# Performance work log

Hardware: AMD Instinct MI355X
Metric: run time of the kernel (lower is better)

## Reference

```python
import jax, jax.numpy as jnp
import numpy as np

WS = 7          # window size
NH = 12         # num heads
DIM = 384
HD = DIM // NH  # head dim = 32
EPS = 1e-5


def _ln(x, g, b):
    m = x.mean(-1, keepdims=True)
    v = ((x - m) ** 2).mean(-1, keepdims=True)
    return (x - m) / jnp.sqrt(v + EPS) * g + b


def _rel_index():
    # exact replica of WindowAttention.__init__ relative_position_index
    coords = np.stack(np.meshgrid(np.arange(WS), np.arange(WS), indexing='ij'))  # (2,ws,ws)
    flat = coords.reshape(2, -1)                                                 # (2,49)
    rel = flat[:, :, None] - flat[:, None, :]                                    # (2,49,49)
    rel = rel.transpose(1, 2, 0).astype(np.int32)
    rel[:, :, 0] += WS - 1
    rel[:, :, 1] += WS - 1
    rel[:, :, 0] *= 2 * WS - 1
    return jnp.asarray(rel.sum(-1))  # (49,49), values in [0, 169)


def setup_inputs() -> dict:
    key = jax.random.key(0)
    ks = jax.random.split(key, 16)
    B, H, W = 16, 56, 56
    L = H * W
    hidden = int(DIM * 4.0)
    p = lambda k, shp: (jax.random.normal(k, shp, jnp.float32) * 0.02)
    return {
        'x': jax.random.normal(ks[0], (B, L, DIM), jnp.float32),
        'kv': jax.random.normal(ks[1], (2, B, NH, WS * WS, HD), jnp.float32),
        'rel_index': _rel_index(),
        'H': H, 'W': W,
        'g1': jnp.ones((DIM,), jnp.float32), 'b1': jnp.zeros((DIM,), jnp.float32),
        'Wqkv': p(ks[2], (DIM, 3 * DIM)), 'bqkv': jnp.zeros((3 * DIM,), jnp.float32),
        'bias_table': p(ks[3], ((2 * WS - 1) ** 2, NH)),
        'Wproj': p(ks[4], (DIM, DIM)), 'bproj': jnp.zeros((DIM,), jnp.float32),
        'g2': jnp.ones((DIM,), jnp.float32), 'b2': jnp.zeros((DIM,), jnp.float32),
        'Wfc1': p(ks[5], (DIM, hidden)), 'bfc1': jnp.zeros((hidden,), jnp.float32),
        'Wfc2': p(ks[6], (hidden, DIM)), 'bfc2': jnp.zeros((DIM,), jnp.float32),
    }


def reference(x, kv, rel_index, H, W, g1, b1, Wqkv, bqkv, bias_table, Wproj, bproj,
              g2, b2, Wfc1, bfc1, Wfc2, bfc2):
    B, L, C = x.shape
    scale = HD ** -0.5
    nWh, nWw = H // WS, W // WS  # H,W divisible by WS -> pad is a no-op; shift_size=0 -> no roll/mask

    h = _ln(x, g1, b1).reshape(B, H, W, C)
    # window_partition -> (B*nW, N, C), N = WS*WS
    hw = h.reshape(B, nWh, WS, nWw, WS, C).transpose(0, 1, 3, 2, 4, 5).reshape(-1, WS * WS, C)
    B_, N, _ = hw.shape

    qkv = (hw @ Wqkv + bqkv).reshape(B_, N, 3, NH, HD).transpose(2, 0, 3, 1, 4)  # (3,B_,nh,N,hd)
    q = qkv[0] * scale
    k, v = kv[0], kv[1]                     # (B, nh, num_kv, hd)
    reps = B_ // k.shape[0]
    k = jnp.repeat(k, reps, axis=0)         # repeat_interleave: each image's windows share its kv
    v = jnp.repeat(v, reps, axis=0)

    attn = jnp.einsum('bhqd,bhkd->bhqk', q, k)                      # (B_,nh,N,N)
    bias = bias_table[rel_index.reshape(-1)].reshape(N, N, NH).transpose(2, 0, 1)
    attn = jax.nn.softmax(attn + bias[None], axis=-1)
    o = jnp.einsum('bhqk,bhkd->bhqd', attn, v)                      # (B_,nh,N,hd)
    o = o.transpose(0, 2, 1, 3).reshape(B_, N, C) @ Wproj + bproj

    # window_reverse -> (B, L, C)
    o = o.reshape(B, nWh, nWw, WS, WS, C).transpose(0, 1, 3, 2, 4, 5).reshape(B, L, C)
    x = x + o
    x = x + (jax.nn.gelu(_ln(x, g2, b2) @ Wfc1 + bfc1, approximate=False) @ Wfc2 + bfc2)
    return x
```

## Files before the change

kernel.cpp:

```cpp
#include <hip/hip_runtime.h>

typedef __attribute__((ext_vector_type(8))) short short8;
typedef __attribute__((ext_vector_type(4))) float floatx4;
typedef unsigned int u32;

#define DIM 384
#define NHEAD 12
#define HDIM 32

__device__ __forceinline__ float bf2f(unsigned int u) {
    union { unsigned int i; float f; } x; x.i = (u & 0xffffu) << 16; return x.f;
}
__device__ __forceinline__ unsigned short f2bf(float f) {
    union { float f; unsigned int i; } x; x.f = f;
    return (unsigned short)((x.i + 0x7fffu + ((x.i >> 16) & 1u)) >> 16);
}

__device__ __forceinline__ int nat2win(int r) {
    int b = r / 3136; int l = r - b * 3136;
    int hh = l / 56, wc = l - hh * 56;
    int wh = hh / 7, nr = hh - wh * 7;
    int ww = wc / 7, nc = wc - ww * 7;
    return ((b << 6) + wh * 8 + ww) * 49 + nr * 7 + nc;
}
__device__ __forceinline__ int win2nat(int r) {
    int w = r / 49; int n = r - w * 49;
    int b = w >> 6; int wi = w & 63;
    int wh = wi >> 3, ww = wi & 7;
    int hh = wh * 7 + n / 7, wc = ww * 7 + n % 7;
    return b * 3136 + hh * 56 + wc;
}

#define GLOAD_LDS16(g, l) \
    __builtin_amdgcn_global_load_lds((const __attribute__((address_space(1))) u32*)(g), \
                                     (__attribute__((address_space(3))) u32*)(l), 16, 0, 0)

#define LDS_U32(p) ((u32)(uintptr_t)(__attribute__((address_space(3))) unsigned short*)(p))

template <int OFF>
__device__ __forceinline__ short8 ds_read128(u32 addr) {
    short8 r;
    asm volatile("ds_read_b128 %0, %1 offset:%2" : "=v"(r) : "v"(addr), "i"(OFF));
    return r;
}

__global__ void transpose_kernel(const float* __restrict__ src,
                                 unsigned short* __restrict__ dst,
                                 int K, int N, int ld) {
    int i = blockIdx.x * blockDim.x + threadIdx.x;
    if (i >= K * N) return;
    int n = i / K, k = i - n * K;
    dst[i] = f2bf(src[(size_t)k * ld + n]);
}

__global__ void bias_expand_kernel(const int* __restrict__ rel_index,
                                   const float* __restrict__ bias_table,
                                   float* __restrict__ biasx) {
    int i = blockIdx.x * blockDim.x + threadIdx.x;
    if (i >= NHEAD * 49 * 49) return;
    int h = i / 2401, r = i - h * 2401;
    biasx[i] = bias_table[rel_index[r] * NHEAD + h];
}

__global__ __launch_bounds__(64) void ln_kernel(const float* __restrict__ x,
                                                const float* __restrict__ g,
                                                const float* __restrict__ b,
                                                unsigned short* __restrict__ out,
                                                int windowed) {
    int r = blockIdx.x;
    int lane = threadIdx.x;
    const float* row = x + (size_t)r * DIM;
    float v[6];
    float s = 0.f, ss = 0.f;
#pragma unroll
    for (int j = 0; j < 3; j++) {
        int c = lane + j * 64;
        float2 f = *(const float2*)(row + 2 * c);
        v[2 * j] = f.x; v[2 * j + 1] = f.y;
        s += f.x + f.y; ss += f.x * f.x + f.y * f.y;
    }
#pragma unroll
    for (int m = 1; m < 64; m <<= 1) {
        s += __shfl_xor(s, m);
        ss += __shfl_xor(ss, m);
    }
    float mean = s * (1.f / DIM);
    float var = ss * (1.f / DIM) - mean * mean;
    float rstd = rsqrtf(var + 1e-5f);
    int orow = windowed ? nat2win(r) : r;
    unsigned short* op = out + (size_t)orow * DIM;
#pragma unroll
    for (int j = 0; j < 3; j++) {
        int c = lane + j * 64;
        float2 gg = *(const float2*)(g + 2 * c);
        float2 bb = *(const float2*)(b + 2 * c);
        float o0 = (v[2 * j] - mean) * rstd * gg.x + bb.x;
        float o1 = (v[2 * j + 1] - mean) * rstd * gg.y + bb.y;
        unsigned int w = ((unsigned int)f2bf(o1) << 16) | f2bf(o0);
        *(unsigned int*)(op + 2 * c) = w;
    }
}

__global__ __launch_bounds__(256) void attn_kernel(const unsigned short* __restrict__ q,
                                                   const float* __restrict__ kv,
                                                   const float* __restrict__ biasx,
                                                   unsigned short* __restrict__ o) {
    __shared__ alignas(16) unsigned short Ks[64 * 40];
    __shared__ alignas(16) unsigned short Vt[32 * 72];
    __shared__ float Bi[49 * 52];
    __shared__ alignas(16) unsigned short Ps[4][16 * 72];

    int blk = blockIdx.x;
    int b = blk / 48; int rem = blk - b * 48;
    int h = rem >> 2; int g = rem & 3;
    size_t row_base = (size_t)(b * 64 + g * 16) * 49;

    int t = threadIdx.x;
    int lane = t & 63;
    int wv = t >> 6;
    int lr = lane & 15;
    int lg = lane >> 4;

    const float* kptr = kv + (size_t)(b * NHEAD + h) * 1568;
    for (int idx = t; idx < 392; idx += 256) {
        int row = idx >> 3, seg = idx & 7;
        float4 f = *(const float4*)(kptr + row * 32 + seg * 4);
        ushort4 h4; h4.x = f2bf(f.x); h4.y = f2bf(f.y); h4.z = f2bf(f.z); h4.w = f2bf(f.w);
        *(ushort4*)&Ks[row * 40 + seg * 4] = h4;
    }
    const float* vptr = kv + (size_t)(192 + b * NHEAD + h) * 1568;
    for (int idx = t; idx < 784; idx += 256) {
        int m = idx >> 4, dp = idx & 15;
        float2 f = *(const float2*)(vptr + m * 32 + dp * 2);
        Vt[(2 * dp) * 72 + m]     = f2bf(f.x);
        Vt[(2 * dp + 1) * 72 + m] = f2bf(f.y);
    }
    for (int idx = t; idx < 32 * 23; idx += 256) {
        int d = idx / 23, m = 49 + idx - d * 23;
        Vt[d * 72 + m] = 0;
    }
    const float* bh = biasx + h * 2401;
    for (int idx = t; idx < 2401; idx += 256) {
        int qr = idx / 49, k = idx - qr * 49;
        Bi[qr * 52 + k] = bh[idx];
    }
    __syncthreads();

    short8 bfr[4], vbf[2][2];
#pragma unroll
    for (int ni = 0; ni < 4; ni++)
        bfr[ni] = *(const short8*)&Ks[(ni * 16 + lr) * 40 + lg * 8];
#pragma unroll
    for (int ni = 0; ni < 2; ni++)
#pragma unroll
        for (int ks = 0; ks < 2; ks++)
            vbf[ni][ks] = *(const short8*)&Vt[(ni * 16 + lr) * 72 + ks * 32 + lg * 8];

    const unsigned short* qb = q + row_base * DIM + h * 32 + lg * 8;
    unsigned short* ob = o + row_base * DIM + h * 32;

    short8 af = *(const short8*)(qb + (size_t)(wv * 16 + lr) * DIM);
    for (int tm = wv; tm < 49; tm += 4) {
        short8 af_next;
        if (tm + 4 < 49) af_next = *(const short8*)(qb + (size_t)((tm + 4) * 16 + lr) * DIM);

        floatx4 sfrag[4];
#pragma unroll
        for (int ni = 0; ni < 4; ni++)
            sfrag[ni] = __builtin_amdgcn_mfma_f32_16x16x32_bf16(af, bfr[ni], (floatx4)0.f, 0, 0, 0);

#pragma unroll
        for (int reg = 0; reg < 4; reg++) {
            int r_loc = tm * 16 + lg * 4 + reg;
            int qr = r_loc % 49;
            float mx = -1e30f;
#pragma unroll
            for (int ni = 0; ni < 4; ni++) {
                int k = ni * 16 + lr;
                float s = sfrag[ni][reg];
                if (k < 49) s += Bi[qr * 52 + k];
                else s = -1e30f;
                sfrag[ni][reg] = s;
                mx = fmaxf(mx, s);
            }
#pragma unroll
            for (int j = 1; j < 16; j <<= 1) mx = fmaxf(mx, __shfl_xor(mx, j));
            float sum = 0.f;
#pragma unroll
            for (int ni = 0; ni < 4; ni++) {
                float e = __expf(sfrag[ni][reg] - mx);
                sfrag[ni][reg] = e;
                sum += e;
            }
#pragma unroll
            for (int j = 1; j < 16; j <<= 1) sum += __shfl_xor(sum, j);
            float inv = 1.f / sum;
#pragma unroll
            for (int ni = 0; ni < 4; ni++)
                Ps[wv][(lg * 4 + reg) * 72 + ni * 16 + lr] = f2bf(sfrag[ni][reg] * inv);
        }
        floatx4 ofrag[2] = {(floatx4)0.f, (floatx4)0.f};
#pragma unroll
        for (int ks = 0; ks < 2; ks++) {
            short8 paf = *(const short8*)&Ps[wv][lr * 72 + ks * 32 + lg * 8];
#pragma unroll
            for (int ni = 0; ni < 2; ni++)
                ofrag[ni] = __builtin_amdgcn_mfma_f32_16x16x32_bf16(paf, vbf[ni][ks], ofrag[ni], 0, 0, 0);
        }
#pragma unroll
        for (int reg = 0; reg < 4; reg++) {
            size_t rg = (size_t)(tm * 16 + lg * 4 + reg) * DIM;
#pragma unroll
            for (int ni = 0; ni < 2; ni++)
                ob[rg + ni * 16 + lr] = f2bf(ofrag[ni][reg]);
        }
        af = af_next;
    }
}

template <int DO_GELU, int DO_REMAP, int OUT_BF16>
__global__ __launch_bounds__(256) void gemm_kernel(const unsigned short* __restrict__ A,
                                                   const unsigned short* __restrict__ Bt,
                                                   const float* __restrict__ bias,
                                                   const float* __restrict__ res,
                                                   void* __restrict__ outv,
                                                   int M, int N, int K, float scale) {
    __shared__ alignas(16) unsigned short As[3][128 * 32];
    __shared__ alignas(16) unsigned short Bs[2][128 * 32];

    int nwg = gridDim.x * gridDim.y;
    int lid = blockIdx.y * gridDim.x + blockIdx.x;
    int q8 = nwg >> 3, r8 = nwg & 7;
    int xcd = lid & 7, pos = lid >> 3;
    int nlid = (xcd < r8 ? xcd * (q8 + 1) : r8 * (q8 + 1) + (xcd - r8) * q8) + pos;
    int m0 = (nlid / gridDim.x) * 128;
    int n0 = (nlid % gridDim.x) * 128;

    int t = threadIdx.x;
    int lane = t & 63;
    int wv = t >> 6;
    int wm = (wv >> 1) * 64, wn = (wv & 1) * 64;
    int lr = lane & 15;
    int lq = lane >> 4;

    int rowS = t >> 2;
    int pcS = t & 3;
    int xrS = (rowS & 3) ^ ((rowS >> 2) & 3);
    int gcS = ((pcS ^ xrS) << 3);

    int xrR = (lr & 3) ^ ((lr >> 2) & 3);
    int swB = ((lq ^ xrR) << 4);

    floatx4 acc[4][4];
#pragma unroll
    for (int i = 0; i < 4; i++)
#pragma unroll
        for (int j = 0; j < 4; j++) acc[i][j] = (floatx4)0.f;

    const unsigned short* Abase = A + (size_t)(m0 + rowS) * K + gcS;
    const unsigned short* Bbase = Bt + (size_t)(n0 + rowS) * K + gcS;
    size_t rstep = (size_t)64 * K;

    auto stageA = [&](int buf, int kk) {
        GLOAD_LDS16(Abase + kk, &As[buf][t * 8]);
        GLOAD_LDS16(Abase + rstep + kk, &As[buf][(256 + t) * 8]);
    };
    auto stageB = [&](int buf, int kk) {
        GLOAD_LDS16(Bbase + kk, &Bs[buf][t * 8]);
        GLOAD_LDS16(Bbase + rstep + kk, &Bs[buf][(256 + t) * 8]);
    };

    u32 asBase = LDS_U32(&As[0][0]);
    u32 bsBase = LDS_U32(&Bs[0][0]);
    u32 aRow = (u32)(((wm + lr) * 64)) + (u32)swB;
    u32 bRow = (u32)(((wn + lr) * 64)) + (u32)swB;

    const int nk = K >> 5;

    stageB(0, 0);
    stageA(0, 0);
    stageA(1, 32);

    for (int kt = 0; kt < nk; ++kt) {
        int ab = kt % 3;
        int bb = kt & 1;
        if (kt + 1 < nk) asm volatile("s_waitcnt vmcnt(2)" ::: "memory");
        else             asm volatile("s_waitcnt vmcnt(0)" ::: "memory");
        __builtin_amdgcn_s_barrier();
        if (kt + 1 < nk) stageB(bb ^ 1, (kt + 1) << 5);
        if (kt + 2 < nk) stageA((kt + 2) % 3, (kt + 2) << 5);

        u32 aB = asBase + (u32)ab * 8192u + aRow;
        u32 bB = bsBase + (u32)bb * 8192u + bRow;

        short8 a0[4], b0[4];
        a0[0] = ds_read128<0>(aB);    a0[1] = ds_read128<1024>(aB);
        a0[2] = ds_read128<2048>(aB); a0[3] = ds_read128<3072>(aB);
        b0[0] = ds_read128<0>(bB);    b0[1] = ds_read128<1024>(bB);
        b0[2] = ds_read128<2048>(bB); b0[3] = ds_read128<3072>(bB);

        asm volatile("s_waitcnt lgkmcnt(0)" ::: "memory");
        __builtin_amdgcn_sched_barrier(0);
        __builtin_amdgcn_s_setprio(1);
#pragma unroll
        for (int i = 0; i < 4; i++)
#pragma unroll
            for (int j = 0; j < 4; j++)
                acc[i][j] = __builtin_amdgcn_mfma_f32_16x16x32_bf16(a0[i], b0[j], acc[i][j], 0, 0, 0);
        __builtin_amdgcn_s_setprio(0);
    }

#pragma unroll
    for (int j = 0; j < 4; j++) {
        int gcol = n0 + wn + j * 16 + lr;
        float bv = bias[gcol];
#pragma unroll
        for (int i = 0; i < 4; i++) {
#pragma unroll
            for (int r = 0; r < 4; r++) {
                int grow = m0 + wm + i * 16 + lq * 4 + r;
                float val = acc[i][j][r] + bv;
                if (DO_GELU) val = 0.5f * val * (1.f + erff(val * 0.70710678118654752f));
                val *= scale;
                int orow = DO_REMAP ? win2nat(grow) : grow;
                size_t idx = (size_t)orow * N + gcol;
                if (res) val += res[idx];
                if (OUT_BF16) ((unsigned short*)outv)[idx] = f2bf(val);
                else          ((float*)outv)[idx] = val;
            }
        }
    }
}

extern "C" void kernel_launch(void* const* d_in, const int* in_sizes, int n_in,
                              void* d_out, int out_size, void* d_ws, size_t ws_size,
                              hipStream_t stream) {
    const float* x          = (const float*)d_in[0];
    const float* kv         = (const float*)d_in[1];
    const int*   rel_index  = (const int*)d_in[2];
    const float* g1         = (const float*)d_in[5];
    const float* b1         = (const float*)d_in[6];
    const float* Wqkv       = (const float*)d_in[7];
    const float* bqkv       = (const float*)d_in[8];
    const float* bias_table = (const float*)d_in[9];
    const float* Wproj      = (const float*)d_in[10];
    const float* bproj      = (const float*)d_in[11];
    const float* g2         = (const float*)d_in[12];
    const float* b2         = (const float*)d_in[13];
    const float* Wfc1       = (const float*)d_in[14];
    const float* bfc1       = (const float*)d_in[15];
    const float* Wfc2       = (const float*)d_in[16];
    const float* bfc2       = (const float*)d_in[17];
    float* out = (float*)d_out;

    char* ws = (char*)d_ws;
    unsigned short* wq_t   = (unsigned short*)(ws);
    unsigned short* wp_t   = (unsigned short*)(ws + 294912);
    unsigned short* wfc1_t = (unsigned short*)(ws + 589824);
    unsigned short* wfc2_t = (unsigned short*)(ws + 1769472);
    float*          biasx  = (float*)(ws + 2949120);
    unsigned short* bufA   = (unsigned short*)(ws + 3080192);
    unsigned short* bufB   = (unsigned short*)(ws + 3080192 + 38535168);

    const int M = 50176;
    const float scale = 0.17677669529663687f;
    const int full_mlp = (ws_size >= (size_t)3080192 + 38535168 + 154140672);

    transpose_kernel<<<(384 * 384 + 255) / 256, 256, 0, stream>>>(Wqkv, wq_t, 384, 384, 1152);
    transpose_kernel<<<(384 * 384 + 255) / 256, 256, 0, stream>>>(Wproj, wp_t, 384, 384, 384);
    transpose_kernel<<<(384 * 1536 + 255) / 256, 256, 0, stream>>>(Wfc1, wfc1_t, 384, 1536, 1536);
    transpose_kernel<<<(1536 * 384 + 255) / 256, 256, 0, stream>>>(Wfc2, wfc2_t, 1536, 384, 384);
    bias_expand_kernel<<<(NHEAD * 2401 + 255) / 256, 256, 0, stream>>>(rel_index, bias_table, biasx);

    ln_kernel<<<M, 64, 0, stream>>>(x, g1, b1, bufA, 1);
    gemm_kernel<0, 0, 1><<<dim3(3, 392), 256, 0, stream>>>(bufA, wq_t, bqkv, nullptr, bufB,
                                                           M, 384, 384, scale);
    attn_kernel<<<16 * NHEAD * 4, 256, 0, stream>>>(bufB, kv, biasx, bufA);
    gemm_kernel<0, 1, 0><<<dim3(3, 392), 256, 0, stream>>>(bufA, wp_t, bproj, x, d_out,
                                                           M, 384, 384, 1.f);
    ln_kernel<<<M, 64, 0, stream>>>(out, g2, b2, bufA, 0);

    if (full_mlp) {
        gemm_kernel<1, 0, 1><<<dim3(12, 392), 256, 0, stream>>>(bufA, wfc1_t, bfc1,
                                                                nullptr, bufB, M, 1536, 384, 1.f);
        gemm_kernel<0, 0, 0><<<dim3(3, 392), 256, 0, stream>>>(bufB, wfc2_t, bfc2,
                                                               out, out, M, 384, 1536, 1.f);
    } else {
        for (int c = 0; c < 4; c++) {
            size_t ro = (size_t)c * 12544;
            gemm_kernel<1, 0, 1><<<dim3(12, 98), 256, 0, stream>>>(bufA + ro * 384, wfc1_t, bfc1,
                                                                   nullptr, bufB, 12544, 1536, 384, 1.f);
            gemm_kernel<0, 0, 0><<<dim3(3, 98), 256, 0, stream>>>(bufB, wfc2_t, bfc2,
                                                                  out + ro * 384, out + ro * 384,
                                                                  12544, 384, 1536, 1.f);
        }
    }
}
```

Measured before the change: 663.6 us.

## Enlarge GEMM tile to 256x128 with 512 threads and fuse prep kernels

Each GEMM workgroup now covers 256 rows with 8 waves instead of 128 rows with 4 waves, so one staged B tile serves twice as many A rows and B loads per output drop. The separate weight transposes and bias expansion are merged into a single prep launch to save launch overhead. The larger block uses more LDS and halves the number of workgroups, which may lower occupancy or leave the 256-CU device less evenly loaded. The epilogue and wave mapping, partly not visible, must handle 8 waves correctly.

```diff
diff --git a/kernel.cpp b/kernel.cpp
--- a/kernel.cpp
+++ b/kernel.cpp
@@ -44,22 +44,46 @@
     return r;
 }
 
-__global__ void transpose_kernel(const float* __restrict__ src,
-                                 unsigned short* __restrict__ dst,
-                                 int K, int N, int ld) {
+__global__ void prep_kernel(const float* __restrict__ Wqkv,
+                            const float* __restrict__ Wproj,
+                            const float* __restrict__ Wfc1,
+                            const float* __restrict__ Wfc2,
+                            const int* __restrict__ rel_index,
+                            const float* __restrict__ bias_table,
+                            unsigned short* __restrict__ wq_t,
+                            unsigned short* __restrict__ wp_t,
+                            unsigned short* __restrict__ wfc1_t,
+                            unsigned short* __restrict__ wfc2_t,
+                            float* __restrict__ biasx) {
     int i = blockIdx.x * blockDim.x + threadIdx.x;
-    if (i >= K * N) return;
-    int n = i / K, k = i - n * K;
-    dst[i] = f2bf(src[(size_t)k * ld + n]);
-}
-
-__global__ void bias_expand_kernel(const int* __restrict__ rel_index,
-                                   const float* __restrict__ bias_table,
-                                   float* __restrict__ biasx) {
-    int i = blockIdx.x * blockDim.x + threadIdx.x;
-    if (i >= NHEAD * 49 * 49) return;
-    int h = i / 2401, r = i - h * 2401;
-    biasx[i] = bias_table[rel_index[r] * NHEAD + h];
+    if (i < 147456) {
+        int n = i / 384, k = i - n * 384;
+        wq_t[i] = f2bf(Wqkv[(size_t)k * 1152 + n]);
+        return;
+    }
+    i -= 147456;
+    if (i < 147456) {
+        int n = i / 384, k = i - n * 384;
+        wp_t[i] = f2bf(Wproj[(size_t)k * 384 + n]);
+        return;
+    }
+    i -= 147456;
+    if (i < 589824) {
+        int n = i / 384, k = i - n * 384;
+        wfc1_t[i] = f2bf(Wfc1[(size_t)k * 1536 + n]);
+        return;
+    }
+    i -= 589824;
+    if (i < 589824) {
+        int n = i / 1536, k = i - n * 1536;
+        wfc2_t[i] = f2bf(Wfc2[(size_t)k * 384 + n]);
+        return;
+    }
+    i -= 589824;
+    if (i < 28812) {
+        int h = i / 2401, r = i - h * 2401;
+        biasx[i] = bias_table[rel_index[r] * NHEAD + h];
+    }
 }
 
 __global__ __launch_bounds__(64) void ln_kernel(const float* __restrict__ x,
@@ -219,13 +243,13 @@
 }
 
 template <int DO_GELU, int DO_REMAP, int OUT_BF16>
-__global__ __launch_bounds__(256) void gemm_kernel(const unsigned short* __restrict__ A,
+__global__ __launch_bounds__(512) void gemm_kernel(const unsigned short* __restrict__ A,
                                                    const unsigned short* __restrict__ Bt,
                                                    const float* __restrict__ bias,
                                                    const float* __restrict__ res,
                                                    void* __restrict__ outv,
                                                    int M, int N, int K, float scale) {
-    __shared__ alignas(16) unsigned short As[3][128 * 32];
+    __shared__ alignas(16) unsigned short As[3][256 * 32];
     __shared__ alignas(16) unsigned short Bs[2][128 * 32];
 
     int nwg = gridDim.x * gridDim.y;
@@ -233,13 +257,14 @@
     int q8 = nwg >> 3, r8 = nwg & 7;
     int xcd = lid & 7, pos = lid >> 3;
     int nlid = (xcd < r8 ? xcd * (q8 + 1) : r8 * (q8 + 1) + (xcd - r8) * q8) + pos;
-    int m0 = (nlid / gridDim.x) * 128;
+    int m0 = (nlid / gridDim.x) * 256;
     int n0 = (nlid % gridDim.x) * 128;
 
     int t = threadIdx.x;
     int lane = t & 63;
     int wv = t >> 6;
-    int wm = (wv >> 1) * 64, wn = (wv & 1) * 64;
+    int wm = (wv >> 1) * 64;
+    int wn = (wv & 1) * 64;
     int lr = lane & 15;
     int lq = lane >> 4;
 
@@ -249,7 +274,7 @@
     int gcS = ((pcS ^ xrS) << 3);
 
     int xrR = (lr & 3) ^ ((lr >> 2) & 3);
-    int swB = ((lq ^ xrR) << 4);
+    u32 swB = (u32)((lq ^ xrR) << 4);
 
     floatx4 acc[4][4];
 #pragma unroll
@@ -259,21 +284,20 @@
 
     const unsigned short* Abase = A + (size_t)(m0 + rowS) * K + gcS;
     const unsigned short* Bbase = Bt + (size_t)(n0 + rowS) * K + gcS;
-    size_t rstep = (size_t)64 * K;
+    size_t arstep = (size_t)128 * K;
 
     auto stageA = [&](int buf, int kk) {
         GLOAD_LDS16(Abase + kk, &As[buf][t * 8]);
-        GLOAD_LDS16(Abase + rstep + kk, &As[buf][(256 + t) * 8]);
+        GLOAD_LDS16(Abase + arstep + kk, &As[buf][(512 + t) * 8]);
     };
     auto stageB = [&](int buf, int kk) {
         GLOAD_LDS16(Bbase + kk, &Bs[buf][t * 8]);
-        GLOAD_LDS16(Bbase + rstep + kk, &Bs[buf][(256 + t) * 8]);
     };
 
     u32 asBase = LDS_U32(&As[0][0]);
     u32 bsBase = LDS_U32(&Bs[0][0]);
-    u32 aRow = (u32)(((wm + lr) * 64)) + (u32)swB;
-    u32 bRow = (u32)(((wn + lr) * 64)) + (u32)swB;
+    u32 aRow = (u32)((wm + lr) * 64) + swB;
+    u32 bRow = (u32)((wn + lr) * 64) + swB;
 
     const int nk = K >> 5;
 
@@ -290,7 +314,7 @@
         if (kt + 1 < nk) stageB(bb ^ 1, (kt + 1) << 5);
         if (kt + 2 < nk) stageA((kt + 2) % 3, (kt + 2) << 5);
 
-        u32 aB = asBase + (u32)ab * 8192u + aRow;
+        u32 aB = asBase + (u32)ab * 16384u + aRow;
         u32 bB = bsBase + (u32)bb * 8192u + bRow;
 
         short8 a0[4], b0[4];
@@ -366,31 +390,29 @@
     const float scale = 0.17677669529663687f;
     const int full_mlp = (ws_size >= (size_t)3080192 + 38535168 + 154140672);
 
-    transpose_kernel<<<(384 * 384 + 255) / 256, 256, 0, stream>>>(Wqkv, wq_t, 384, 384, 1152);
-    transpose_kernel<<<(384 * 384 + 255) / 256, 256, 0, stream>>>(Wproj, wp_t, 384, 384, 384);
-    transpose_kernel<<<(384 * 1536 + 255) / 256, 256, 0, stream>>>(Wfc1, wfc1_t, 384, 1536, 1536);
-    transpose_kernel<<<(1536 * 384 + 255) / 256, 256, 0, stream>>>(Wfc2, wfc2_t, 1536, 384, 384);
-    bias_expand_kernel<<<(NHEAD * 2401 + 255) / 256, 256, 0, stream>>>(rel_index, bias_table, biasx);
+    prep_kernel<<<(1503372 + 255) / 256, 256, 0, stream>>>(Wqkv, Wproj, Wfc1, Wfc2,
+                                                           rel_index, bias_table,
+                                                           wq_t, wp_t, wfc1_t, wfc2_t, biasx);
 
     ln_kernel<<<M, 64, 0, stream>>>(x, g1, b1, bufA, 1);
-    gemm_kernel<0, 0, 1><<<dim3(3, 392), 256, 0, stream>>>(bufA, wq_t, bqkv, nullptr, bufB,
-                                                           M, 384, 384, scale);
+    gemm_kernel<0, 0, 1><<<dim3(3, M / 256), 512, 0, stream>>>(bufA, wq_t, bqkv, nullptr, bufB,
+                                                               M, 384, 384, scale);
     attn_kernel<<<16 * NHEAD * 4, 256, 0, stream>>>(bufB, kv, biasx, bufA);
-    gemm_kernel<0, 1, 0><<<dim3(3, 392), 256, 0, stream>>>(bufA, wp_t, bproj, x, d_out,
-                                                           M, 384, 384, 1.f);
+    gemm_kernel<0, 1, 0><<<dim3(3, M / 256), 512, 0, stream>>>(bufA, wp_t, bproj, x, d_out,
+                                                               M, 384, 384, 1.f);
     ln_kernel<<<M, 64, 0, stream>>>(out, g2, b2, bufA, 0);
 
     if (full_mlp) {
-        gemm_kernel<1, 0, 1><<<dim3(12, 392), 256, 0, stream>>>(bufA, wfc1_t, bfc1,
-                                                                nullptr, bufB, M, 1536, 384, 1.f);
-        gemm_kernel<0, 0, 0><<<dim3(3, 392), 256, 0, stream>>>(bufB, wfc2_t, bfc2,
-                                                               out, out, M, 384, 1536, 1.f);
+        gemm_kernel<1, 0, 1><<<dim3(12, M / 256), 512, 0, stream>>>(bufA, wfc1_t, bfc1,
+                                                                    nullptr, bufB, M, 1536, 384, 1.f);
+        gemm_kernel<0, 0, 0><<<dim3(3, M / 256), 512, 0, stream>>>(bufB, wfc2_t, bfc2,
+                                                                   out, out, M, 384, 1536, 1.f);
     } else {
         for (int c = 0; c < 4; c++) {
             size_t ro = (size_t)c * 12544;
-            gemm_kernel<1, 0, 1><<<dim3(12, 98), 256, 0, stream>>>(bufA + ro * 384, wfc1_t, bfc1,
+            gemm_kernel<1, 0, 1><<<dim3(12, 49), 512, 0, stream>>>(bufA + ro * 384, wfc1_t, bfc1,
                                                                    nullptr, bufB, 12544, 1536, 384, 1.f);
-            gemm_kernel<0, 0, 0><<<dim3(3, 98), 256, 0, stream>>>(bufB, wfc2_t, bfc2,
+            gemm_kernel<0, 0, 0><<<dim3(3, 49), 512, 0, stream>>>(bufB, wfc2_t, bfc2,
                                                                   out + ro * 384, out + ro * 384,
                                                                   12544, 384, 1536, 1.f);
         }
```

Result: faster. 603.4 us (-9.1%).
